# Kernel optimization log

Measured on AMD Instinct MI355X. Metric: run time of the kernel, lower is better.

## Reference

```python
import jax, jax.numpy as jnp
import numpy as np
from jax import lax

B, S, D = 2, 1024, 1024
N = 16            # mamba state dim
EXPAND = 2
DI = EXPAND * D   # inner dim 2048
K = 4             # depthwise conv kernel
H = 16            # soliton heads
DH = D // H
DT_RANK = D // 16
SOL_DT = 0.1      # soliton integration step


def _ln(x, g, b):
    mu = jnp.mean(x, -1, keepdims=True)
    var = jnp.var(x, -1, keepdims=True)
    return (x - mu) / jnp.sqrt(var + 1e-5) * g + b


def setup_inputs() -> dict:
    key = jax.random.key(0)
    ks = jax.random.split(key, 12)
    def nrm(k, sh, sc=0.02):
        return jax.random.normal(k, sh, jnp.float32) * sc
    return {
        'x': nrm(ks[0], (B, S, D), 1.0),
        'ln1_g': jnp.ones(D), 'ln1_b': jnp.zeros(D),
        'W_in': nrm(ks[1], (D, 2 * DI)), 'b_in': jnp.zeros(2 * DI),
        'conv_w': nrm(ks[2], (DI, K), 0.1), 'conv_b': jnp.zeros(DI),
        'W_xp': nrm(ks[3], (DI, DT_RANK + 2 * N)),
        'W_dt': nrm(ks[4], (DT_RANK, DI), 0.1),
        'b_dt': jnp.full((DI,), -4.6),  # softplus(-4.6) ~ 0.01 init dt
        'A_log': jnp.log(jnp.broadcast_to(jnp.arange(1, N + 1, dtype=jnp.float32), (DI, N))),
        'D_skip': jnp.ones(DI),
        'W_out': nrm(ks[5], (DI, D)), 'b_out': jnp.zeros(D),
        'ln2_g': jnp.ones(D), 'ln2_b': jnp.zeros(D),
        'W_si': nrm(ks[6], (D, D)), 'b_si': jnp.zeros(D),
        'gates': nrm(ks[7], (H, 3), 0.1),   # per-head weights for [sine-Gordon, KdV, Heimburg-Jackson]
        'alpha': nrm(ks[8], (H,), 0.1),     # HJ nonlinearity coefficient
        'W_so': nrm(ks[9], (D, D)), 'b_so': jnp.zeros(D),
    }


def _forward(x, ln1_g, ln1_b, W_in, b_in, conv_w, conv_b, W_xp, W_dt, b_dt,
             A_log, D_skip, W_out, b_out, ln2_g, ln2_b, W_si, b_si,
             gates, alpha, W_so, b_so):
    b, s, d = x.shape
    # ---- Mamba mixer branch ----
    u = _ln(x, ln1_g, ln1_b)
    xz = u @ W_in + b_in                                   # [b,s,2*DI]
    xp, z = jnp.split(xz, 2, axis=-1)                      # [b,s,DI] each
    # causal depthwise conv along sequence
    xt = xp.transpose(0, 2, 1)                             # [b,DI,s]
    yc = lax.conv_general_dilated(xt, conv_w[:, None, :], (1,), [(K - 1, 0)],
                                  feature_group_count=DI,
                                  dimension_numbers=('NCW', 'OIW', 'NCW'))
    xc = jax.nn.silu(yc.transpose(0, 2, 1) + conv_b)       # [b,s,DI]
    dbc = xc @ W_xp
    dtr, Bs, Cs = jnp.split(dbc, [DT_RANK, DT_RANK + N], axis=-1)
    dt = jax.nn.softplus(dtr @ W_dt + b_dt)                # [b,s,DI]
    A = -jnp.exp(A_log)                                    # [DI,N]
    dA = jnp.exp(dt[..., None] * A)                        # [b,s,DI,N]
    dBx = (dt * xc)[..., None] * Bs[:, :, None, :]         # [b,s,DI,N]

    def step(h, inp):
        dA_t, dBx_t, C_t = inp
        h = dA_t * h + dBx_t                               # [b,DI,N]
        y = jnp.einsum('bdn,bn->bd', h, C_t)
        return h, y

    h0 = jnp.zeros((b, DI, N), x.dtype)
    xs = (dA.transpose(1, 0, 2, 3), dBx.transpose(1, 0, 2, 3), Cs.transpose(1, 0, 2))
    _, ys = lax.scan(step, h0, xs)
    y = ys.transpose(1, 0, 2)                              # [b,s,DI]
    y = (y + xc * D_skip) * jax.nn.silu(z)
    x = x + y @ W_out + b_out

    # ---- Soliton interaction branch ----
    v = _ln(x, ln2_g, ln2_b)
    uu = (v @ W_si + b_si).reshape(b, s, H, DH)
    up = jnp.pad(uu, ((0, 0), (2, 2), (0, 0), (0, 0)), mode='edge')
    ux = (up[:, 3:-1] - up[:, 1:-3]) * 0.5                 # central 1st derivative
    uxx = up[:, 3:-1] - 2.0 * uu + up[:, 1:-3]
    uxxx = (up[:, 4:] - 2.0 * up[:, 3:-1] + 2.0 * up[:, 1:-3] - up[:, :-4]) * 0.5
    sg = jnp.sin(uu)                                       # sine-Gordon
    kdv = -6.0 * uu * ux - uxxx                            # KdV
    hj = (1.0 + alpha[None, None, :, None] * uu) * uxx     # Heimburg-Jackson
    du = (gates[None, None, :, 0:1] * sg
          + gates[None, None, :, 1:2] * kdv
          + gates[None, None, :, 2:3] * hj)
    sol = (SOL_DT * du).reshape(b, s, d) @ W_so + b_so
    return x + sol


def reference(x, ln1_g, ln1_b, W_in, b_in, conv_w, conv_b, W_xp, W_dt, b_dt,
              A_log, D_skip, W_out, b_out, ln2_g, ln2_b, W_si, b_si,
              gates, alpha, W_so, b_so):
    return _forward(x, ln1_g, ln1_b, W_in, b_in, conv_w, conv_b, W_xp, W_dt, b_dt,
                    A_log, D_skip, W_out, b_out, ln2_g, ln2_b, W_si, b_si,
                    gates, alpha, W_so, b_so)
```

## Files before the change

### kernel.cpp

```cpp
#include <hip/hip_runtime.h>
#include <hip/hip_bf16.h>
#include <math.h>

typedef unsigned short u16;
typedef unsigned int u32;
typedef __attribute__((ext_vector_type(8))) short short8;
typedef __attribute__((ext_vector_type(4))) float f32x4;

constexpr int CB = 2;
constexpr int CS = 1024;
constexpr int CD = 1024;
constexpr int CDI = 2048;
constexpr int CNC2 = 64;
constexpr int CL2 = 16;

__device__ inline u16 f2bf(float v) {
  __hip_bfloat16 h = __float2bfloat16(v);
  return *reinterpret_cast<u16*>(&h);
}
__device__ inline float bf2f(u16 v) {
  return __uint_as_float(((u32)v) << 16);
}

__device__ inline void gload16(const void* g, void* l) {
  __builtin_amdgcn_global_load_lds((const __attribute__((address_space(1))) void*)g,
                                   (__attribute__((address_space(3))) void*)l, 16, 0, 0);
}

__global__ __launch_bounds__(256)
void transpose_bf16_kernel(const float* __restrict__ in, u16* __restrict__ out,
                           int K, int N, int Npad) {
  __shared__ float tile[32][33];
  int n0 = blockIdx.x * 32, k0 = blockIdx.y * 32;
  int tx = threadIdx.x & 31, ty = threadIdx.x >> 5;
#pragma unroll
  for (int i = 0; i < 4; ++i) {
    int k = k0 + ty + i * 8, n = n0 + tx;
    tile[ty + i * 8][tx] = (n < N) ? in[(size_t)k * N + n] : 0.f;
  }
  __syncthreads();
#pragma unroll
  for (int i = 0; i < 4; ++i) {
    int n = n0 + ty + i * 8, k = k0 + tx;
    out[(size_t)n * K + k] = f2bf(tile[tx][ty + i * 8]);
  }
}

__global__ __launch_bounds__(256)
void ln_kernel(const float* __restrict__ x, const float* __restrict__ g,
               const float* __restrict__ bb, u16* __restrict__ outb) {
  int row = blockIdx.x;
  const float4* xr = (const float4*)(x + (size_t)row * CD);
  float4 v = xr[threadIdx.x];
  float s = v.x + v.y + v.z + v.w;
  float ss = v.x * v.x + v.y * v.y + v.z * v.z + v.w * v.w;
#pragma unroll
  for (int o = 1; o < 64; o <<= 1) { s += __shfl_xor(s, o); ss += __shfl_xor(ss, o); }
  __shared__ float sb[4], ssb[4];
  int wid = threadIdx.x >> 6;
  if ((threadIdx.x & 63) == 0) { sb[wid] = s; ssb[wid] = ss; }
  __syncthreads();
  s = sb[0] + sb[1] + sb[2] + sb[3];
  ss = ssb[0] + ssb[1] + ssb[2] + ssb[3];
  float mu = s * (1.f / CD);
  float var = ss * (1.f / CD) - mu * mu;
  float rstd = rsqrtf(var + 1e-5f);
  float4 gv = ((const float4*)g)[threadIdx.x];
  float4 bv = ((const float4*)bb)[threadIdx.x];
  ushort4 o;
  o.x = f2bf((v.x - mu) * rstd * gv.x + bv.x);
  o.y = f2bf((v.y - mu) * rstd * gv.y + bv.y);
  o.z = f2bf((v.z - mu) * rstd * gv.z + bv.z);
  o.w = f2bf((v.w - mu) * rstd * gv.w + bv.w);
  ((ushort4*)(outb + (size_t)row * CD))[threadIdx.x] = o;
}

template<int BN>
__global__ __launch_bounds__(256)
void gemm_bf16_kernel(const u16* __restrict__ A, int lda,
                      const u16* __restrict__ Bt, int ldb,
                      const float* __restrict__ bias,
                      const float* __restrict__ resid, int ldr,
                      float* __restrict__ C, int ldc,
                      u16* __restrict__ aux, int auxN,
                      int Nact, int K, int act) {
  constexpr int WN = BN / 32;
  __shared__ __align__(16) u16 As[2 * 128 * 64];
  __shared__ __align__(16) u16 Bs[2 * BN * 64];
  const int tid = threadIdx.x, lane = tid & 63, wid = tid >> 6;
  const int wr = wid >> 1, wc = wid & 1;
  int nwg = gridDim.x * gridDim.y;
  int bid = blockIdx.y * gridDim.x + blockIdx.x;
  int swz = (bid & 7) * (nwg >> 3) + (bid >> 3);
  int bx = swz % gridDim.x, by = swz / gridDim.x;
  const int bm = by * 128, bn = bx * BN;
  const int ksegs = gridDim.z;
  const int kper = K / ksegs;
  const int kbeg = blockIdx.z * kper;
  const int nt = kper / 64;
  f32x4 acc[4][WN] = {};

  auto stage = [&](int t, int buf) {
    int k0 = kbeg + t * 64;
    u16* Ad = As + buf * (128 * 64);
    u16* Bd = Bs + buf * (BN * 64);
#pragma unroll
    for (int j = 0; j < 4; ++j) {
      int cbase = j * 256 + wid * 64;
      int c = cbase + lane;
      int row = c >> 3;
      int kc = (c & 7) ^ (row & 7);
      gload16(A + (size_t)(bm + row) * lda + k0 + kc * 8, Ad + cbase * 8);
    }
#pragma unroll
    for (int j = 0; j < BN / 32; ++j) {
      int cbase = j * 256 + wid * 64;
      int c = cbase + lane;
      int row = c >> 3;
      int kc = (c & 7) ^ (row & 7);
      gload16(Bt + (size_t)(bn + row) * ldb + k0 + kc * 8, Bd + cbase * 8);
    }
  };

  stage(0, 0);
  __syncthreads();
  int cur = 0;
  for (int t = 0; t < nt; ++t) {
    if (t + 1 < nt) stage(t + 1, cur ^ 1);
    const u16* Asb = As + cur * (128 * 64);
    const u16* Bsb = Bs + cur * (BN * 64);
#pragma unroll
    for (int ks = 0; ks < 64; ks += 32) {
      short8 af[4], bfr[WN];
#pragma unroll
      for (int m = 0; m < 4; ++m) {
        int r = wr * 64 + m * 16 + (lane & 15);
        int ch = (lane >> 4) + (ks >> 3);
        af[m] = *(const short8*)&Asb[r * 64 + ((ch ^ (r & 7)) << 3)];
      }
#pragma unroll
      for (int n = 0; n < WN; ++n) {
        int r = wc * (BN / 2) + n * 16 + (lane & 15);
        int ch = (lane >> 4) + (ks >> 3);
        bfr[n] = *(const short8*)&Bsb[r * 64 + ((ch ^ (r & 7)) << 3)];
      }
#pragma unroll
      for (int m = 0; m < 4; ++m)
#pragma unroll
        for (int n = 0; n < WN; ++n)
          acc[m][n] = __builtin_amdgcn_mfma_f32_16x16x32_bf16(af[m], bfr[n], acc[m][n], 0, 0, 0);
    }
    __syncthreads();
    cur ^= 1;
  }

  const int fr = lane & 15, fq = lane >> 4;
#pragma unroll
  for (int m = 0; m < 4; ++m) {
#pragma unroll
    for (int n = 0; n < WN; ++n) {
#pragma unroll
      for (int j = 0; j < 4; ++j) {
        int row = bm + wr * 64 + m * 16 + fq * 4 + j;
        int col = bn + wc * (BN / 2) + n * 16 + fr;
        if (col < Nact) {
          float v = acc[m][n][j];
          if (ksegs == 1) {
            if (bias) v += bias[col];
            if (resid) v += resid[(size_t)row * ldr + col];
            if (act == 1) v = (v > 20.f) ? v : log1pf(__expf(v));
            if (C) C[(size_t)row * ldc + col] = v;
            if (aux && col < auxN) aux[(size_t)row * auxN + col] = f2bf(v);
          } else {
            atomicAdd(&C[(size_t)row * ldc + col], v);
          }
        }
      }
    }
  }
}

__global__ __launch_bounds__(256)
void conv_silu_kernel(const u16* __restrict__ xz, const float* __restrict__ w,
                      const float* __restrict__ cb, u16* __restrict__ xcb) {
  int idx = blockIdx.x * 256 + threadIdx.x;
  int d = idx & (CDI - 1);
  int t = (idx >> 11) & (CS - 1);
  int b = idx >> 21;
  const u16* col = xz + (size_t)b * CS * 4096 + d;
  float acc = cb[d];
#pragma unroll
  for (int k = 0; k < 4; ++k) {
    int tt = t - 3 + k;
    if (tt >= 0) acc = fmaf(bf2f(col[(size_t)tt * 4096]), w[d * 4 + k], acc);
  }
  float v = acc * (1.f / (1.f + __expf(-acc)));
  xcb[idx] = f2bf(v);
}

__global__ __launch_bounds__(256)
void dtr_convert_kernel(const float* __restrict__ dbc, u16* __restrict__ dtrb) {
  int idx = blockIdx.x * 256 + threadIdx.x;
  int r = idx >> 6, k = idx & 63;
  dtrb[idx] = f2bf(dbc[r * 96 + k]);
}

__global__ __launch_bounds__(256)
void scan1_kernel(const u16* __restrict__ dtb, const u16* __restrict__ xcb,
                  const float* __restrict__ dbc, const float* __restrict__ A_log,
                  u16* __restrict__ P, u16* __restrict__ Q) {
  int gid = blockIdx.x * 256 + threadIdx.x;
  int d = gid & (CDI - 1);
  int c = (gid >> 11) & (CNC2 - 1);
  int b = gid >> 17;
  float acoef[16];
#pragma unroll
  for (int j = 0; j < 4; ++j) {
    float4 al = ((const float4*)(A_log + d * 16))[j];
    acoef[j * 4 + 0] = -__expf(al.x);
    acoef[j * 4 + 1] = -__expf(al.y);
    acoef[j * 4 + 2] = -__expf(al.z);
    acoef[j * 4 + 3] = -__expf(al.w);
  }
  float Pv[16], Qv[16];
#pragma unroll
  for (int n = 0; n < 16; ++n) { Pv[n] = 1.f; Qv[n] = 0.f; }
  size_t rowbase = (size_t)b * CS + (size_t)c * CL2;
  for (int i = 0; i < CL2; ++i) {
    size_t r = rowbase + i;
    float dtv = bf2f(dtb[r * CDI + d]);
    float xcv = bf2f(xcb[r * CDI + d]);
    float dx = dtv * xcv;
    const float4* bs4 = (const float4*)(dbc + r * 96 + 64);
    float bs[16];
#pragma unroll
    for (int j = 0; j < 4; ++j) {
      float4 t4 = bs4[j];
      bs[j * 4 + 0] = t4.x; bs[j * 4 + 1] = t4.y; bs[j * 4 + 2] = t4.z; bs[j * 4 + 3] = t4.w;
    }
#pragma unroll
    for (int n = 0; n < 16; ++n) {
      float a = __expf(dtv * acoef[n]);
      Pv[n] *= a;
      Qv[n] = fmaf(a, Qv[n], dx * bs[n]);
    }
  }
  size_t o = (((size_t)b * CNC2 + c) * CDI + d) * 16;
  u16 pb[16], qb[16];
#pragma unroll
  for (int n = 0; n < 16; ++n) { pb[n] = f2bf(Pv[n]); qb[n] = f2bf(Qv[n]); }
#pragma unroll
  for (int j = 0; j < 2; ++j) {
    *(short8*)(P + o + j * 8) = *(short8*)(pb + j * 8);
    *(short8*)(Q + o + j * 8) = *(short8*)(qb + j * 8);
  }
}

__global__ __launch_bounds__(256)
void scan2_kernel(const u16* __restrict__ P, u16* __restrict__ Q) {
  int gid = blockIdx.x * 256 + threadIdx.x;
  int n = gid & 15;
  int d = (gid >> 4) & (CDI - 1);
  int b = gid >> 15;
  float h = 0.f;
  for (int c = 0; c < CNC2; ++c) {
    size_t o = (((size_t)b * CNC2 + c) * CDI + d) * 16 + n;
    float p = bf2f(P[o]), q = bf2f(Q[o]);
    Q[o] = f2bf(h);
    h = fmaf(p, h, q);
  }
}

__global__ __launch_bounds__(256)
void scan3_kernel(const u16* __restrict__ dtb, const u16* __restrict__ xcb,
                  const float* __restrict__ dbc, const float* __restrict__ A_log,
                  const u16* __restrict__ Q, const u16* __restrict__ xz,
                  const float* __restrict__ Dskip, u16* __restrict__ y2b) {
  int gid = blockIdx.x * 256 + threadIdx.x;
  int d = gid & (CDI - 1);
  int c = (gid >> 11) & (CNC2 - 1);
  int b = gid >> 17;
  float acoef[16];
#pragma unroll
  for (int j = 0; j < 4; ++j) {
    float4 al = ((const float4*)(A_log + d * 16))[j];
    acoef[j * 4 + 0] = -__expf(al.x);
    acoef[j * 4 + 1] = -__expf(al.y);
    acoef[j * 4 + 2] = -__expf(al.z);
    acoef[j * 4 + 3] = -__expf(al.w);
  }
  float h[16];
  size_t o = (((size_t)b * CNC2 + c) * CDI + d) * 16;
#pragma unroll
  for (int j = 0; j < 2; ++j) {
    short8 q8 = *(const short8*)(Q + o + j * 8);
#pragma unroll
    for (int n = 0; n < 8; ++n) h[j * 8 + n] = bf2f((u16)q8[n]);
  }
  float dsk = Dskip[d];
  size_t rowbase = (size_t)b * CS + (size_t)c * CL2;
  for (int i = 0; i < CL2; ++i) {
    size_t r = rowbase + i;
    float dtv = bf2f(dtb[r * CDI + d]);
    float xcv = bf2f(xcb[r * CDI + d]);
    float zv = bf2f(xz[r * 4096 + 2048 + d]);
    float dx = dtv * xcv;
    const float4* bc4 = (const float4*)(dbc + r * 96 + 64);
    float bs[16], cs[16];
#pragma unroll
    for (int j = 0; j < 4; ++j) {
      float4 t4 = bc4[j];
      bs[j * 4 + 0] = t4.x; bs[j * 4 + 1] = t4.y; bs[j * 4 + 2] = t4.z; bs[j * 4 + 3] = t4.w;
      float4 u4 = bc4[4 + j];
      cs[j * 4 + 0] = u4.x; cs[j * 4 + 1] = u4.y; cs[j * 4 + 2] = u4.z; cs[j * 4 + 3] = u4.w;
    }
    float y = 0.f;
#pragma unroll
    for (int n = 0; n < 16; ++n) {
      float a = __expf(dtv * acoef[n]);
      h[n] = fmaf(a, h[n], dx * bs[n]);
      y = fmaf(h[n], cs[n], y);
    }
    float sz = zv * (1.f / (1.f + __expf(-zv)));
    y2b[r * CDI + d] = f2bf((y + xcv * dsk) * sz);
  }
}

__global__ __launch_bounds__(256)
void soliton_kernel(const float* __restrict__ uu, const float* __restrict__ gates,
                    const float* __restrict__ alpha, u16* __restrict__ sol) {
  int idx = blockIdx.x * 256 + threadIdx.x;
  int d = idx & (CD - 1);
  int t = (idx >> 10) & (CS - 1);
  int b = idx >> 20;
  int h = d >> 6;
  const float* base = uu + (size_t)b * CS * CD + d;
  int tm2 = max(t - 2, 0), tm1 = max(t - 1, 0);
  int tp1 = min(t + 1, CS - 1), tp2 = min(t + 2, CS - 1);
  float um2 = base[(size_t)tm2 * CD];
  float um1 = base[(size_t)tm1 * CD];
  float u0  = base[(size_t)t   * CD];
  float up1 = base[(size_t)tp1 * CD];
  float up2 = base[(size_t)tp2 * CD];
  float ux   = (up1 - um1) * 0.5f;
  float uxx  = up1 - 2.f * u0 + um1;
  float uxxx = (up2 - 2.f * up1 + 2.f * um1 - um2) * 0.5f;
  float sg = sinf(u0);
  float kdv = -6.f * u0 * ux - uxxx;
  float hj = (1.f + alpha[h] * u0) * uxx;
  float du = gates[h * 3 + 0] * sg + gates[h * 3 + 1] * kdv + gates[h * 3 + 2] * hj;
  sol[idx] = f2bf(0.1f * du);
}

extern "C" void kernel_launch(void* const* d_in, const int* in_sizes, int n_in,
                              void* d_out, int out_size, void* d_ws, size_t ws_size,
                              hipStream_t stream) {
  const float* x      = (const float*)d_in[0];
  const float* ln1_g  = (const float*)d_in[1];
  const float* ln1_b  = (const float*)d_in[2];
  const float* W_in   = (const float*)d_in[3];
  const float* b_in   = (const float*)d_in[4];
  const float* conv_w = (const float*)d_in[5];
  const float* conv_b = (const float*)d_in[6];
  const float* W_xp   = (const float*)d_in[7];
  const float* W_dt   = (const float*)d_in[8];
  const float* b_dt   = (const float*)d_in[9];
  const float* A_log  = (const float*)d_in[10];
  const float* D_skip = (const float*)d_in[11];
  const float* W_out  = (const float*)d_in[12];
  const float* b_out  = (const float*)d_in[13];
  const float* ln2_g  = (const float*)d_in[14];
  const float* ln2_b  = (const float*)d_in[15];
  const float* W_si   = (const float*)d_in[16];
  const float* b_si   = (const float*)d_in[17];
  const float* gates  = (const float*)d_in[18];
  const float* alpha  = (const float*)d_in[19];
  const float* W_so   = (const float*)d_in[20];
  const float* b_so   = (const float*)d_in[21];
  float* out = (float*)d_out;

  float* ws = (float*)d_ws;
  size_t off = 0;
  auto alloc = [&](size_t nwords) { float* p = ws + off; off += nwords; return p; };
  const size_t BS = (size_t)CB * CS;
  const size_t M1 = 1024 * 1024;

  u16* Wt_in  = (u16*)alloc(2 * M1);
  u16* Wt_xp  = (u16*)alloc(128 * 1024);
  u16* Wt_dt  = (u16*)alloc(64 * 1024);
  u16* Wt_out = (u16*)alloc(M1);
  u16* Wt_si  = (u16*)alloc(M1 / 2);
  u16* Wt_so  = (u16*)alloc(M1 / 2);
  u16* u_bf   = (u16*)alloc(M1);
  u16* sol_bf = u_bf;
  u16* xz_bf  = (u16*)alloc(4 * M1);
  u16* dt_bf  = (u16*)alloc(2 * M1);
  u16* xc_bf  = (u16*)alloc(2 * M1);
  float* dbc  = alloc(BS * 96);
  u16* dtr_bf = (u16*)alloc(64 * 1024);
  u16* Pb     = (u16*)alloc(2 * M1);
  u16* Qb     = (u16*)alloc(2 * M1);
  u16* y2_bf  = (u16*)alloc(2 * M1);
  float* uu   = (float*)Pb;

  dim3 blk(256);

  transpose_bf16_kernel<<<dim3(128, 32), blk, 0, stream>>>(W_in, Wt_in, 1024, 4096, 4096);
  transpose_bf16_kernel<<<dim3(4, 64), blk, 0, stream>>>(W_xp, Wt_xp, 2048, 96, 128);
  transpose_bf16_kernel<<<dim3(64, 2), blk, 0, stream>>>(W_dt, Wt_dt, 64, 2048, 2048);
  transpose_bf16_kernel<<<dim3(32, 64), blk, 0, stream>>>(W_out, Wt_out, 2048, 1024, 1024);
  transpose_bf16_kernel<<<dim3(32, 32), blk, 0, stream>>>(W_si, Wt_si, 1024, 1024, 1024);
  transpose_bf16_kernel<<<dim3(32, 32), blk, 0, stream>>>(W_so, Wt_so, 1024, 1024, 1024);

  ln_kernel<<<BS, blk, 0, stream>>>(x, ln1_g, ln1_b, u_bf);
  gemm_bf16_kernel<128><<<dim3(32, 16), blk, 0, stream>>>(u_bf, 1024, Wt_in, 1024, b_in, nullptr, 0,
                                                          nullptr, 0, xz_bf, 4096, 4096, 1024, 0);
  conv_silu_kernel<<<(BS * CDI) / 256, blk, 0, stream>>>(xz_bf, conv_w, conv_b, xc_bf);
  hipMemsetAsync(dbc, 0, BS * 96 * sizeof(float), stream);
  gemm_bf16_kernel<128><<<dim3(1, 16, 8), blk, 0, stream>>>(xc_bf, 2048, Wt_xp, 2048, nullptr, nullptr, 0,
                                                            dbc, 96, nullptr, 0, 96, 2048, 0);
  dtr_convert_kernel<<<(BS * 64) / 256, blk, 0, stream>>>(dbc, dtr_bf);
  gemm_bf16_kernel<128><<<dim3(16, 16), blk, 0, stream>>>(dtr_bf, 64, Wt_dt, 64, b_dt, nullptr, 0,
                                                          nullptr, 0, dt_bf, 2048, 2048, 64, 1);
  scan1_kernel<<<(CB * CNC2 * CDI) / 256, blk, 0, stream>>>(dt_bf, xc_bf, dbc, A_log, Pb, Qb);
  scan2_kernel<<<(CB * CDI * 16) / 256, blk, 0, stream>>>(Pb, Qb);
  scan3_kernel<<<(CB * CNC2 * CDI) / 256, blk, 0, stream>>>(dt_bf, xc_bf, dbc, A_log, Qb, xz_bf, D_skip, y2_bf);
  gemm_bf16_kernel<64><<<dim3(16, 16), blk, 0, stream>>>(y2_bf, 2048, Wt_out, 2048, b_out, x, 1024,
                                                         out, CD, nullptr, 0, 1024, 2048, 0);
  ln_kernel<<<BS, blk, 0, stream>>>(out, ln2_g, ln2_b, u_bf);
  gemm_bf16_kernel<64><<<dim3(16, 16), blk, 0, stream>>>(u_bf, 1024, Wt_si, 1024, b_si, nullptr, 0,
                                                         uu, CD, nullptr, 0, 1024, 1024, 0);
  soliton_kernel<<<(BS * CD) / 256, blk, 0, stream>>>(uu, gates, alpha, sol_bf);
  gemm_bf16_kernel<64><<<dim3(16, 16), blk, 0, stream>>>(sol_bf, 1024, Wt_so, 1024, b_so, out, 1024,
                                                         out, CD, nullptr, 0, 1024, 1024, 0);
}
```

Before: 284.2 us.

## Merge weight transposes into one launch, specialize GEMM strides, batch scan2 loads

```diff
diff --git a/kernel.cpp b/kernel.cpp
--- a/kernel.cpp
+++ b/kernel.cpp
@@ -27,22 +27,30 @@
                                    (__attribute__((address_space(3))) void*)l, 16, 0, 0);
 }
 
-__global__ __launch_bounds__(256)
-void transpose_bf16_kernel(const float* __restrict__ in, u16* __restrict__ out,
-                           int K, int N, int Npad) {
+struct TJob { const float* src; u16* dst; int K, N, gx, base; };
+struct TJobs { TJob j[6]; };
+
+__global__ __launch_bounds__(256)
+void transpose_all_kernel(TJobs jobs) {
+  int b = blockIdx.x;
+  int ji = 0;
+#pragma unroll
+  for (int i = 1; i < 6; ++i) if (b >= jobs.j[i].base) ji = i;
+  TJob jb = jobs.j[ji];
+  int lb = b - jb.base;
+  int n0 = (lb % jb.gx) * 32, k0 = (lb / jb.gx) * 32;
   __shared__ float tile[32][33];
-  int n0 = blockIdx.x * 32, k0 = blockIdx.y * 32;
   int tx = threadIdx.x & 31, ty = threadIdx.x >> 5;
 #pragma unroll
   for (int i = 0; i < 4; ++i) {
     int k = k0 + ty + i * 8, n = n0 + tx;
-    tile[ty + i * 8][tx] = (n < N) ? in[(size_t)k * N + n] : 0.f;
+    tile[ty + i * 8][tx] = (n < jb.N) ? jb.src[(size_t)k * jb.N + n] : 0.f;
   }
   __syncthreads();
 #pragma unroll
   for (int i = 0; i < 4; ++i) {
     int n = n0 + ty + i * 8, k = k0 + tx;
-    out[(size_t)n * K + k] = f2bf(tile[tx][ty + i * 8]);
+    jb.dst[(size_t)n * jb.K + k] = f2bf(tile[tx][ty + i * 8]);
   }
 }
 
@@ -75,18 +83,19 @@
   ((ushort4*)(outb + (size_t)row * CD))[threadIdx.x] = o;
 }
 
-template<int BN>
-__global__ __launch_bounds__(256)
-void gemm_bf16_kernel(const u16* __restrict__ A, int lda,
-                      const u16* __restrict__ Bt, int ldb,
-                      const float* __restrict__ bias,
-                      const float* __restrict__ resid, int ldr,
-                      float* __restrict__ C, int ldc,
-                      u16* __restrict__ aux, int auxN,
-                      int Nact, int K, int act) {
+template<int BN, int LDA, int LDB>
+__global__ __launch_bounds__(256)
+void gemm2_kernel(const u16* __restrict__ A, const u16* __restrict__ Bt,
+                  const float* __restrict__ bias,
+                  const float* __restrict__ resid, int ldr,
+                  float* __restrict__ C, int ldc,
+                  u16* __restrict__ aux, int auxN,
+                  int Nact, int K, int act) {
   constexpr int WN = BN / 32;
-  __shared__ __align__(16) u16 As[2 * 128 * 64];
-  __shared__ __align__(16) u16 Bs[2 * BN * 64];
+  constexpr int AHALF = 128 * 64;
+  constexpr int BHALF = BN * 64;
+  __shared__ __align__(16) u16 As[2 * AHALF];
+  __shared__ __align__(16) u16 Bs[2 * BHALF];
   const int tid = threadIdx.x, lane = tid & 63, wid = tid >> 6;
   const int wr = wid >> 1, wc = wid & 1;
   int nwg = gridDim.x * gridDim.y;
@@ -94,67 +103,79 @@
   int swz = (bid & 7) * (nwg >> 3) + (bid >> 3);
   int bx = swz % gridDim.x, by = swz / gridDim.x;
   const int bm = by * 128, bn = bx * BN;
-  const int ksegs = gridDim.z;
-  const int kper = K / ksegs;
+  const int kper = K / gridDim.z;
   const int kbeg = blockIdx.z * kper;
   const int nt = kper / 64;
+
+  int a_src[4], b_src[WN], a_dst[4], b_dst[WN];
+#pragma unroll
+  for (int j = 0; j < 4; ++j) {
+    int c = tid + j * 256;
+    int row = c >> 3, kc = (c & 7) ^ (row & 7);
+    a_src[j] = (bm + row) * LDA + kc * 8 + kbeg;
+    a_dst[j] = (j * 256 + wid * 64) * 8;
+  }
+#pragma unroll
+  for (int j = 0; j < WN; ++j) {
+    int c = tid + j * 256;
+    int row = c >> 3, kc = (c & 7) ^ (row & 7);
+    b_src[j] = (bn + row) * LDB + kc * 8 + kbeg;
+    b_dst[j] = (j * 256 + wid * 64) * 8;
+  }
+  int afo[4], bfo[WN];
+#pragma unroll
+  for (int m = 0; m < 4; ++m) {
+    int r = wr * 64 + m * 16 + (lane & 15);
+    afo[m] = r * 64 + (((lane >> 4) ^ (r & 7)) << 3);
+  }
+#pragma unroll
+  for (int n = 0; n < WN; ++n) {
+    int r = wc * (BN / 2) + n * 16 + (lane & 15);
+    bfo[n] = r * 64 + (((lane >> 4) ^ (r & 7)) << 3);
+  }
   f32x4 acc[4][WN] = {};
 
-  auto stage = [&](int t, int buf) {
-    int k0 = kbeg + t * 64;
-    u16* Ad = As + buf * (128 * 64);
-    u16* Bd = Bs + buf * (BN * 64);
-#pragma unroll
-    for (int j = 0; j < 4; ++j) {
-      int cbase = j * 256 + wid * 64;
-      int c = cbase + lane;
-      int row = c >> 3;
-      int kc = (c & 7) ^ (row & 7);
-      gload16(A + (size_t)(bm + row) * lda + k0 + kc * 8, Ad + cbase * 8);
-    }
-#pragma unroll
-    for (int j = 0; j < BN / 32; ++j) {
-      int cbase = j * 256 + wid * 64;
-      int c = cbase + lane;
-      int row = c >> 3;
-      int kc = (c & 7) ^ (row & 7);
-      gload16(Bt + (size_t)(bn + row) * ldb + k0 + kc * 8, Bd + cbase * 8);
-    }
+  auto stage = [&](int t, int abuf, int bbuf) {
+    int k0 = t * 64;
+#pragma unroll
+    for (int j = 0; j < 4; ++j)
+      gload16(A + a_src[j] + k0, As + abuf + a_dst[j]);
+#pragma unroll
+    for (int j = 0; j < WN; ++j)
+      gload16(Bt + b_src[j] + k0, Bs + bbuf + b_dst[j]);
   };
-
-  stage(0, 0);
-  __syncthreads();
-  int cur = 0;
-  for (int t = 0; t < nt; ++t) {
-    if (t + 1 < nt) stage(t + 1, cur ^ 1);
-    const u16* Asb = As + cur * (128 * 64);
-    const u16* Bsb = Bs + cur * (BN * 64);
-#pragma unroll
-    for (int ks = 0; ks < 64; ks += 32) {
+  auto compute = [&](int abuf, int bbuf) {
+#pragma unroll
+    for (int ks = 0; ks < 2; ++ks) {
       short8 af[4], bfr[WN];
 #pragma unroll
-      for (int m = 0; m < 4; ++m) {
-        int r = wr * 64 + m * 16 + (lane & 15);
-        int ch = (lane >> 4) + (ks >> 3);
-        af[m] = *(const short8*)&Asb[r * 64 + ((ch ^ (r & 7)) << 3)];
-      }
-#pragma unroll
-      for (int n = 0; n < WN; ++n) {
-        int r = wc * (BN / 2) + n * 16 + (lane & 15);
-        int ch = (lane >> 4) + (ks >> 3);
-        bfr[n] = *(const short8*)&Bsb[r * 64 + ((ch ^ (r & 7)) << 3)];
-      }
+      for (int m = 0; m < 4; ++m) af[m] = *(const short8*)&As[abuf + (afo[m] ^ (ks * 32))];
+#pragma unroll
+      for (int n = 0; n < WN; ++n) bfr[n] = *(const short8*)&Bs[bbuf + (bfo[n] ^ (ks * 32))];
 #pragma unroll
       for (int m = 0; m < 4; ++m)
 #pragma unroll
         for (int n = 0; n < WN; ++n)
           acc[m][n] = __builtin_amdgcn_mfma_f32_16x16x32_bf16(af[m], bfr[n], acc[m][n], 0, 0, 0);
     }
+  };
+
+  stage(0, 0, 0);
+  __syncthreads();
+  int t = 0;
+  while (true) {
+    if (t + 1 < nt) stage(t + 1, AHALF, BHALF);
+    compute(0, 0);
     __syncthreads();
-    cur ^= 1;
+    if (++t == nt) break;
+    if (t + 1 < nt) stage(t + 1, 0, 0);
+    compute(AHALF, BHALF);
+    __syncthreads();
+    if (++t == nt) break;
   }
 
   const int fr = lane & 15, fq = lane >> 4;
+  const int ksegs = gridDim.z;
 #pragma unroll
   for (int m = 0; m < 4; ++m) {
 #pragma unroll
@@ -262,12 +283,23 @@
   int n = gid & 15;
   int d = (gid >> 4) & (CDI - 1);
   int b = gid >> 15;
+  int obase = ((b * CNC2) * CDI + d) * 16 + n;
+  constexpr int CSTRIDE = CDI * 16;
   float h = 0.f;
-  for (int c = 0; c < CNC2; ++c) {
-    size_t o = (((size_t)b * CNC2 + c) * CDI + d) * 16 + n;
-    float p = bf2f(P[o]), q = bf2f(Q[o]);
-    Q[o] = f2bf(h);
-    h = fmaf(p, h, q);
+  for (int c0 = 0; c0 < CNC2; c0 += 8) {
+    float pv[8], qv[8];
+#pragma unroll
+    for (int i = 0; i < 8; ++i) {
+      int o = obase + (c0 + i) * CSTRIDE;
+      pv[i] = bf2f(P[o]);
+      qv[i] = bf2f(Q[o]);
+    }
+#pragma unroll
+    for (int i = 0; i < 8; ++i) {
+      int o = obase + (c0 + i) * CSTRIDE;
+      Q[o] = f2bf(h);
+      h = fmaf(pv[i], h, qv[i]);
+    }
   }
 }
 
@@ -405,32 +437,44 @@
 
   dim3 blk(256);
 
-  transpose_bf16_kernel<<<dim3(128, 32), blk, 0, stream>>>(W_in, Wt_in, 1024, 4096, 4096);
-  transpose_bf16_kernel<<<dim3(4, 64), blk, 0, stream>>>(W_xp, Wt_xp, 2048, 96, 128);
-  transpose_bf16_kernel<<<dim3(64, 2), blk, 0, stream>>>(W_dt, Wt_dt, 64, 2048, 2048);
-  transpose_bf16_kernel<<<dim3(32, 64), blk, 0, stream>>>(W_out, Wt_out, 2048, 1024, 1024);
-  transpose_bf16_kernel<<<dim3(32, 32), blk, 0, stream>>>(W_si, Wt_si, 1024, 1024, 1024);
-  transpose_bf16_kernel<<<dim3(32, 32), blk, 0, stream>>>(W_so, Wt_so, 1024, 1024, 1024);
+  {
+    TJobs jobs;
+    int base = 0;
+    auto mk = [&](const float* s, u16* dst, int K, int N) {
+      int gx = (N + 31) / 32, gy = K / 32;
+      TJob j{s, dst, K, N, gx, base};
+      base += gx * gy;
+      return j;
+    };
+    jobs.j[0] = mk(W_in, Wt_in, 1024, 4096);
+    jobs.j[1] = mk(W_xp, Wt_xp, 2048, 96);
+    jobs.j[2] = mk(W_dt, Wt_dt, 64, 2048);
+    jobs.j[3] = mk(W_out, Wt_out, 2048, 1024);
+    jobs.j[4] = mk(W_si, Wt_si, 1024, 1024);
+    jobs.j[5] = mk(W_so, Wt_so, 1024, 1024);
+    hipMemsetAsync(Wt_xp, 0, 128 * 2048 * sizeof(u16), stream);
+    transpose_all_kernel<<<base, blk, 0, stream>>>(jobs);
+  }
 
   ln_kernel<<<BS, blk, 0, stream>>>(x, ln1_g, ln1_b, u_bf);
-  gemm_bf16_kernel<128><<<dim3(32, 16), blk, 0, stream>>>(u_bf, 1024, Wt_in, 1024, b_in, nullptr, 0,
-                                                          nullptr, 0, xz_bf, 4096, 4096, 1024, 0);
+  gemm2_kernel<128, 1024, 1024><<<dim3(32, 16), blk, 0, stream>>>(
+      u_bf, Wt_in, b_in, nullptr, 0, nullptr, 0, xz_bf, 4096, 4096, 1024, 0);
   conv_silu_kernel<<<(BS * CDI) / 256, blk, 0, stream>>>(xz_bf, conv_w, conv_b, xc_bf);
   hipMemsetAsync(dbc, 0, BS * 96 * sizeof(float), stream);
-  gemm_bf16_kernel<128><<<dim3(1, 16, 8), blk, 0, stream>>>(xc_bf, 2048, Wt_xp, 2048, nullptr, nullptr, 0,
-                                                            dbc, 96, nullptr, 0, 96, 2048, 0);
+  gemm2_kernel<128, 2048, 2048><<<dim3(1, 16, 8), blk, 0, stream>>>(
+      xc_bf, Wt_xp, nullptr, nullptr, 0, dbc, 96, nullptr, 0, 96, 2048, 0);
   dtr_convert_kernel<<<(BS * 64) / 256, blk, 0, stream>>>(dbc, dtr_bf);
-  gemm_bf16_kernel<128><<<dim3(16, 16), blk, 0, stream>>>(dtr_bf, 64, Wt_dt, 64, b_dt, nullptr, 0,
-                                                          nullptr, 0, dt_bf, 2048, 2048, 64, 1);
+  gemm2_kernel<128, 64, 64><<<dim3(16, 16), blk, 0, stream>>>(
+      dtr_bf, Wt_dt, b_dt, nullptr, 0, nullptr, 0, dt_bf, 2048, 2048, 64, 1);
   scan1_kernel<<<(CB * CNC2 * CDI) / 256, blk, 0, stream>>>(dt_bf, xc_bf, dbc, A_log, Pb, Qb);
   scan2_kernel<<<(CB * CDI * 16) / 256, blk, 0, stream>>>(Pb, Qb);
   scan3_kernel<<<(CB * CNC2 * CDI) / 256, blk, 0, stream>>>(dt_bf, xc_bf, dbc, A_log, Qb, xz_bf, D_skip, y2_bf);
-  gemm_bf16_kernel<64><<<dim3(16, 16), blk, 0, stream>>>(y2_bf, 2048, Wt_out, 2048, b_out, x, 1024,
-                                                         out, CD, nullptr, 0, 1024, 2048, 0);
+  gemm2_kernel<64, 2048, 2048><<<dim3(16, 16), blk, 0, stream>>>(
+      y2_bf, Wt_out, b_out, x, 1024, out, CD, nullptr, 0, 1024, 2048, 0);
   ln_kernel<<<BS, blk, 0, stream>>>(out, ln2_g, ln2_b, u_bf);
-  gemm_bf16_kernel<64><<<dim3(16, 16), blk, 0, stream>>>(u_bf, 1024, Wt_si, 1024, b_si, nullptr, 0,
-                                                         uu, CD, nullptr, 0, 1024, 1024, 0);
+  gemm2_kernel<64, 1024, 1024><<<dim3(16, 16), blk, 0, stream>>>(
+      u_bf, Wt_si, b_si, nullptr, 0, uu, CD, nullptr, 0, 1024, 1024, 0);
   soliton_kernel<<<(BS * CD) / 256, blk, 0, stream>>>(uu, gates, alpha, sol_bf);
-  gemm_bf16_kernel<64><<<dim3(16, 16), blk, 0, stream>>>(sol_bf, 1024, Wt_so, 1024, b_so, out, 1024,
-                                                         out, CD, nullptr, 0, 1024, 1024, 0);
-}
+  gemm2_kernel<64, 1024, 1024><<<dim3(16, 16), blk, 0, stream>>>(
+      sol_bf, Wt_so, b_so, out, 1024, out, CD, nullptr, 0, 1024, 1024, 0);
+}
```

Result: no change. 286.8 us (+0.9%).
